# Kernel optimization log

Measured on AMD Instinct MI355X. Metric: run time of the kernel, lower is better.

## Reference

```python
import jax, jax.numpy as jnp
import numpy as np

B, S, DIM, H, DH, DEPTH, NCLS = 4, 2048, 128, 8, 128, 2, 10
M = 128          # number of FAVOR+ random features
CHUNK = 128      # chunk size for causal linear attention
INNER = H * DH   # performer-pytorch: dim_head=dim -> inner_dim = heads*dim
FF = 4 * DIM


def layernorm(x, g, b, eps=1e-5):
    mu = jnp.mean(x, axis=-1, keepdims=True)
    var = jnp.mean((x - mu) ** 2, axis=-1, keepdims=True)
    return (x - mu) * jax.lax.rsqrt(var + eps) * g + b


def softmax_kernel(data, proj, is_query, eps=1e-4):
    # FAVOR+ positive softmax-kernel features. data: [B,H,S,DH], proj: [M,DH]
    norm = DH ** -0.25
    ratio = M ** -0.5
    d = data * norm
    dd = jnp.einsum('bhsd,md->bhsm', d, proj)
    diag = 0.5 * jnp.sum(d * d, axis=-1, keepdims=True)
    if is_query:
        stab = jnp.max(dd, axis=-1, keepdims=True)
    else:
        stab = jnp.max(dd, axis=(-2, -1), keepdims=True)
    stab = jax.lax.stop_gradient(stab)
    return ratio * (jnp.exp(dd - diag - stab) + eps)


def causal_linear_attention(qp, kp, v):
    # qp,kp: [B,H,S,M], v: [B,H,S,DH]; chunked prefix-sum causal linear attention
    b, h, s, m = qp.shape
    d = v.shape[-1]
    nc = s // CHUNK
    def to_chunks(t):
        return t.reshape(b, h, nc, CHUNK, -1).transpose(2, 0, 1, 3, 4)
    qc, kc, vc = to_chunks(qp), to_chunks(kp), to_chunks(v)
    tri = jnp.tril(jnp.ones((CHUNK, CHUNK), qp.dtype))
    def step(carry, inp):
        kv_sum, k_sum = carry           # [b,h,m,d], [b,h,m]
        qi, ki, vi = inp                # [b,h,CHUNK,*]
        attn = jnp.einsum('bhim,bhjm->bhij', qi, ki) * tri
        num = jnp.einsum('bhij,bhjd->bhid', attn, vi) \
            + jnp.einsum('bhim,bhmd->bhid', qi, kv_sum)
        den = jnp.sum(attn, axis=-1) + jnp.einsum('bhim,bhm->bhi', qi, k_sum)
        out = num / (den[..., None] + 1e-6)
        kv_sum = kv_sum + jnp.einsum('bhjm,bhjd->bhmd', ki, vi)
        k_sum = k_sum + jnp.sum(ki, axis=2)
        return (kv_sum, k_sum), out
    init = (jnp.zeros((b, h, m, d), qp.dtype), jnp.zeros((b, h, m), qp.dtype))
    _, out = jax.lax.scan(step, init, (qc, kc, vc))
    return out.transpose(1, 2, 0, 3, 4).reshape(b, h, s, d)


def setup_inputs():
    key = jax.random.key(0)
    ks = jax.random.split(key, 12)
    rng = np.random.default_rng(0)
    # sinusoidal positional encoding [S, DIM]
    pe = np.zeros((S, DIM), np.float32)
    pos = np.arange(S)[:, None].astype(np.float32)
    div = np.exp(np.arange(0, DIM, 2).astype(np.float32) * (-np.log(10000.0) / DIM))
    pe[:, 0::2] = np.sin(pos * div)
    pe[:, 1::2] = np.cos(pos * div)
    # orthogonal random feature projections per layer [DEPTH, M, DH]
    proj = np.stack([
        (np.linalg.qr(rng.standard_normal((DH, DH)))[0][:M] * np.sqrt(DH))
        for _ in range(DEPTH)
    ]).astype(np.float32)
    def gn(k, shape, scale):
        return jax.random.normal(k, shape, jnp.float32) * scale
    return {
        'x': gn(ks[0], (B, S, 1), 1.0),
        'lin_w': gn(ks[1], (1, DIM), 1.0),
        'lin_b': jnp.zeros((DIM,), jnp.float32),
        'pe': jnp.asarray(pe),
        'proj': jnp.asarray(proj),
        'ln1_g': jnp.ones((DEPTH, DIM), jnp.float32),
        'ln1_b': jnp.zeros((DEPTH, DIM), jnp.float32),
        'wq': gn(ks[2], (DEPTH, DIM, INNER), DIM ** -0.5),
        'wk': gn(ks[3], (DEPTH, DIM, INNER), DIM ** -0.5),
        'wv': gn(ks[4], (DEPTH, DIM, INNER), DIM ** -0.5),
        'wo': gn(ks[5], (DEPTH, INNER, DIM), INNER ** -0.5),
        'wo_b': jnp.zeros((DEPTH, DIM), jnp.float32),
        'ln2_g': jnp.ones((DEPTH, DIM), jnp.float32),
        'ln2_b': jnp.zeros((DEPTH, DIM), jnp.float32),
        'ff1_w': gn(ks[6], (DEPTH, DIM, FF), DIM ** -0.5),
        'ff1_b': jnp.zeros((DEPTH, FF), jnp.float32),
        'ff2_w': gn(ks[7], (DEPTH, FF, DIM), FF ** -0.5),
        'ff2_b': jnp.zeros((DEPTH, DIM), jnp.float32),
        'fin_w': gn(ks[8], (DIM, NCLS), DIM ** -0.5),
        'fin_b': jnp.zeros((NCLS,), jnp.float32),
    }


def reference(x, lin_w, lin_b, pe, proj, ln1_g, ln1_b, wq, wk, wv, wo, wo_b,
              ln2_g, ln2_b, ff1_w, ff1_b, ff2_w, ff2_b, fin_w, fin_b):
    h = x @ lin_w + lin_b            # [B,S,DIM]
    h = h + pe[None]
    for l in range(DEPTH):
        # --- pre-norm FAVOR+ causal self-attention ---
        y = layernorm(h, ln1_g[l], ln1_b[l])
        def split(t):  # [B,S,INNER] -> [B,H,S,DH]
            return t.reshape(B, S, H, DH).transpose(0, 2, 1, 3)
        q, k, v = split(y @ wq[l]), split(y @ wk[l]), split(y @ wv[l])
        qp = softmax_kernel(q, proj[l], True)
        kp = softmax_kernel(k, proj[l], False)
        o = causal_linear_attention(qp, kp, v)          # [B,H,S,DH]
        o = o.transpose(0, 2, 1, 3).reshape(B, S, INNER)
        h = h + (o @ wo[l] + wo_b[l])
        # --- pre-norm FFN ---
        y = layernorm(h, ln2_g[l], ln2_b[l])
        f = jax.nn.gelu(y @ ff1_w[l] + ff1_b[l]) @ ff2_w[l] + ff2_b[l]
        h = h + f
    pooled = jnp.mean(h, axis=1)     # [B,DIM]
    return pooled @ fin_w + fin_b    # [B,NCLS]
```

## Files before the change

kernel.cpp:

```cpp
#include <hip/hip_runtime.h>
#include <hip/hip_bf16.h>

#define Bb 4
#define Ss 2048
#define DIMc 128
#define Hh 8
#define DHc 128
#define Mf 128
#define CH 128
#define NCc 16
#define INNERc 1024
#define FFc 512

union F4 { float4 v; float f[4]; };
typedef unsigned short u16;

typedef __bf16 bf16x8 __attribute__((ext_vector_type(8)));
typedef float  f32x4  __attribute__((ext_vector_type(4)));

__device__ __forceinline__ unsigned fkey(float f){
  unsigned b = __float_as_uint(f);
  return (b & 0x80000000u) ? ~b : (b | 0x80000000u);
}
__device__ __forceinline__ float funkey(unsigned u){
  unsigned b = (u & 0x80000000u) ? (u & 0x7fffffffu) : ~u;
  return __uint_as_float(b);
}
__device__ __forceinline__ float gelu_f(float x){
  return 0.5f*x*(1.0f + tanhf(0.7978845608028654f*(x + 0.044715f*x*x*x)));
}
__device__ __forceinline__ u16 f2bu(float f){
  unsigned u = __float_as_uint(f);
  return (u16)((u + 0x7fffu + ((u>>16)&1u)) >> 16);
}
__device__ __forceinline__ float b2f(u16 u){
  return __uint_as_float(((unsigned)u)<<16);
}

__device__ __forceinline__ bf16x8 ldfrag(const u16* base, int row, int e){
  int byte = (row*256 + e*2) ^ ((row&7)<<4);
  return *(const bf16x8*)((const char*)base + byte);
}
__device__ __forceinline__ void stage_lin_bf(u16* dst, const u16* src, int srs, int t){
  #pragma unroll
  for(int it=0; it<8; ++it){
    int idx = t + it*256; int r = idx>>4, c8 = idx&15;
    int byte = (r*256 + c8*16) ^ ((r&7)<<4);
    *(uint4*)((char*)dst + byte) = *(const uint4*)(src + r*srs + c8*8);
  }
}
__device__ __forceinline__ void stage_lin_bf_s(u16* dst, const u16* src, int srs,
    int t, float sc, float off){
  #pragma unroll
  for(int it=0; it<8; ++it){
    int idx = t + it*256; int r = idx>>4, c8 = idx&15;
    u16 tmp[8]; *(uint4*)tmp = *(const uint4*)(src + r*srs + c8*8);
    #pragma unroll
    for(int u=0;u<8;u++) tmp[u] = f2bu(fmaf(b2f(tmp[u]), sc, off));
    int byte = (r*256 + c8*16) ^ ((r&7)<<4);
    *(uint4*)((char*)dst + byte) = *(uint4*)tmp;
  }
}
__device__ __forceinline__ void stage_lin_f32(u16* dst, const float* src, int srs, int t){
  #pragma unroll
  for(int it=0; it<8; ++it){
    int idx = t + it*256; int r = idx>>4, c8 = idx&15;
    F4 v0, v1;
    v0.v = *(const float4*)(src + r*srs + c8*8);
    v1.v = *(const float4*)(src + r*srs + c8*8 + 4);
    u16 tmp[8];
    #pragma unroll
    for(int u=0;u<4;u++){ tmp[u] = f2bu(v0.f[u]); tmp[4+u] = f2bu(v1.f[u]); }
    int byte = (r*256 + c8*16) ^ ((r&7)<<4);
    *(uint4*)((char*)dst + byte) = *(uint4*)tmp;
  }
}
__device__ __forceinline__ void stage_tr_bf(u16* dst, const u16* src, int srs, int t){
  int j0 = (t & 63)*2; int wv = t>>6;
  #pragma unroll
  for(int it=0; it<2; ++it){
    int d0 = wv*16 + it*64;
    u16 a0[16], a1[16];
    *(uint4*)&a0[0] = *(const uint4*)(src + j0*srs + d0);
    *(uint4*)&a0[8] = *(const uint4*)(src + j0*srs + d0 + 8);
    *(uint4*)&a1[0] = *(const uint4*)(src + (j0+1)*srs + d0);
    *(uint4*)&a1[8] = *(const uint4*)(src + (j0+1)*srs + d0 + 8);
    #pragma unroll
    for(int dc=0; dc<16; ++dc){
      int d = d0 + dc;
      unsigned pk = (unsigned)a0[dc] | ((unsigned)a1[dc]<<16);
      int byte = (d*256 + j0*2) ^ ((d&7)<<4);
      *(unsigned*)((char*)dst + byte) = pk;
    }
  }
}
__device__ __forceinline__ void stage_tr_bf_s(u16* dst, const u16* src, int srs,
    int t, float sc, float off){
  int j0 = (t & 63)*2; int wv = t>>6;
  #pragma unroll
  for(int it=0; it<2; ++it){
    int d0 = wv*16 + it*64;
    u16 a0[16], a1[16];
    *(uint4*)&a0[0] = *(const uint4*)(src + j0*srs + d0);
    *(uint4*)&a0[8] = *(const uint4*)(src + j0*srs + d0 + 8);
    *(uint4*)&a1[0] = *(const uint4*)(src + (j0+1)*srs + d0);
    *(uint4*)&a1[8] = *(const uint4*)(src + (j0+1)*srs + d0 + 8);
    #pragma unroll
    for(int dc=0; dc<16; ++dc){
      int d = d0 + dc;
      unsigned pk = (unsigned)f2bu(fmaf(b2f(a0[dc]), sc, off)) |
                    ((unsigned)f2bu(fmaf(b2f(a1[dc]), sc, off))<<16);
      int byte = (d*256 + j0*2) ^ ((d&7)<<4);
      *(unsigned*)((char*)dst + byte) = pk;
    }
  }
}

__device__ __forceinline__ int2 swz_tile(){
  int nx = gridDim.x;
  int nwg = gridDim.x*gridDim.y;
  int lin = blockIdx.y*nx + blockIdx.x;
  int q = nwg>>3, r = nwg&7;
  int xcd = lin&7, idx = lin>>3;
  int nl = (xcd<r) ? (xcd*(q+1)+idx) : (r*(q+1)+(xcd-r)*q+idx);
  return make_int2(nl % nx, nl / nx);
}

__global__ __launch_bounds__(64) void k_init(unsigned* kstab){
  if(threadIdx.x < 64) kstab[threadIdx.x] = 0u;
}

__global__ __launch_bounds__(256) void k_embed(const float* __restrict__ x,
    const float* __restrict__ lw, const float* __restrict__ lb,
    const float* __restrict__ pe, float* __restrict__ h){
  int idx = blockIdx.x*256 + threadIdx.x;
  int d = idx & 127; int bs = idx >> 7; int s = bs & (Ss-1);
  h[idx] = x[bs]*lw[d] + lb[d] + pe[s*DIMc + d];
}

__global__ __launch_bounds__(256) void k_ln(const float* __restrict__ in,
    const float* __restrict__ g, const float* __restrict__ bta,
    u16* __restrict__ out){
  int wave = threadIdx.x >> 6; int lane = threadIdx.x & 63;
  int row = blockIdx.x*4 + wave;
  const float* r = in + row*DIMc;
  float x1 = r[lane], x2 = r[lane+64];
  float s = x1+x2, sq = x1*x1 + x2*x2;
  #pragma unroll
  for(int m=1;m<64;m<<=1){ s += __shfl_xor(s,m,64); sq += __shfl_xor(sq,m,64); }
  float mu = s * (1.0f/128.0f);
  float var = sq*(1.0f/128.0f) - mu*mu;
  float rs = rsqrtf(var + 1e-5f);
  out[row*DIMc+lane]    = f2bu((x1-mu)*rs*g[lane]+bta[lane]);
  out[row*DIMc+lane+64] = f2bu((x2-mu)*rs*g[lane+64]+bta[lane+64]);
}

template<bool QKV3, bool BIAS, bool GELU>
__global__ __launch_bounds__(256) void k_gemm128(const u16* __restrict__ A,
    const float* __restrict__ B0, const float* __restrict__ B1,
    const float* __restrict__ B2, const float* __restrict__ bias,
    u16* __restrict__ C0, u16* __restrict__ C1, u16* __restrict__ C2,
    int N){
  __shared__ __align__(16) u16 As[16384];
  __shared__ __align__(16) u16 Bs[16384];
  int2 tt = swz_tile();
  int tn = tt.x, m0 = tt.y*128;
  const float* Bw; u16* C; int n0;
  if(QKV3){
    int tpw = N>>7;
    int widx = tn / tpw; n0 = (tn % tpw)*128;
    Bw = (widx==0) ? B0 : ((widx==1) ? B1 : B2);
    C  = (widx==0) ? C0 : ((widx==1) ? C1 : C2);
  } else { Bw = B0; C = C0; n0 = tn*128; }
  int t = threadIdx.x; int lane = t&63, w = t>>6;
  int fr = lane&15, kc = lane>>4;
  stage_lin_bf(As, A + (size_t)m0*128, 128, t);
  {
    #pragma unroll
    for(int it=0; it<8; ++it){
      int idx = t + it*256; int n = idx&127, c8 = idx>>7;
      u16 tmp[8];
      #pragma unroll
      for(int j=0;j<8;j++) tmp[j] = f2bu(Bw[(c8*8+j)*N + n0 + n]);
      int byte = (n*256 + c8*16) ^ ((n&7)<<4);
      *(uint4*)((char*)Bs + byte) = *(uint4*)tmp;
    }
  }
  __syncthreads();
  f32x4 acc[2][8] = {};
  #pragma unroll
  for(int ks=0; ks<4; ++ks){
    bf16x8 a[2];
    #pragma unroll
    for(int i=0;i<2;i++) a[i] = ldfrag(As, w*32+i*16+fr, ks*32+kc*8);
    bf16x8 bm[8];
    #pragma unroll
    for(int cb=0;cb<8;cb++) bm[cb] = ldfrag(Bs, cb*16+fr, ks*32+kc*8);
    #pragma unroll
    for(int i=0;i<2;i++)
      #pragma unroll
      for(int cb=0;cb<8;cb++)
        acc[i][cb] = __builtin_amdgcn_mfma_f32_16x16x32_bf16(a[i], bm[cb], acc[i][cb], 0,0,0);
  }
  #pragma unroll
  for(int i=0;i<2;i++){
    #pragma unroll
    for(int r=0;r<4;r++){
      int row = m0 + w*32 + i*16 + kc*4 + r;
      #pragma unroll
      for(int cb=0;cb<8;cb++){
        int col = n0 + cb*16 + fr;
        float val = acc[i][cb][r];
        if(BIAS) val += bias[col];
        if(GELU) val = gelu_f(val);
        C[(size_t)row*N + col] = f2bu(val);
      }
    }
  }
}

template<bool BIAS, bool GELU, bool RES, bool OBF>
__global__ __launch_bounds__(256) void k_gemm_bf(const u16* __restrict__ A,
    const float* __restrict__ Bw, const float* __restrict__ bias,
    const float* __restrict__ resid, void* __restrict__ Cp, int N, int K){
  __shared__ u16 As[64][40];
  __shared__ u16 Bs[64][40];
  int2 tt = swz_tile();
  int n0 = tt.x*64, m0 = tt.y*64;
  int t = threadIdx.x; int wid = t>>6, lane = t&63;
  int wr = wid>>1, wc = wid&1;
  int fr = lane&15, kc = lane>>4;
  f32x4 acc[2][2] = {};
  for(int k0=0; k0<K; k0+=32){
    {
      int r = t>>2, c8 = t&3;
      *(uint4*)&As[r][c8*8] = *(const uint4*)(A + (m0+r)*K + k0 + c8*8);
    }
    {
      int n = t&63, c8 = t>>6;
      u16 tmp[8];
      #pragma unroll
      for(int j=0;j<8;j++) tmp[j] = f2bu(Bw[(k0 + c8*8 + j)*N + n0 + n]);
      *(uint4*)&Bs[n][c8*8] = *(uint4*)tmp;
    }
    __syncthreads();
    bf16x8 af[2], bf[2];
    #pragma unroll
    for(int i=0;i<2;i++) af[i] = *(const bf16x8*)&As[wr*32 + i*16 + fr][kc*8];
    #pragma unroll
    for(int j=0;j<2;j++) bf[j] = *(const bf16x8*)&Bs[wc*32 + j*16 + fr][kc*8];
    #pragma unroll
    for(int i=0;i<2;i++)
      #pragma unroll
      for(int j=0;j<2;j++)
        acc[i][j] = __builtin_amdgcn_mfma_f32_16x16x32_bf16(af[i], bf[j], acc[i][j], 0, 0, 0);
    __syncthreads();
  }
  #pragma unroll
  for(int i=0;i<2;i++){
    #pragma unroll
    for(int r=0;r<4;r++){
      int row = m0 + wr*32 + i*16 + kc*4 + r;
      #pragma unroll
      for(int j=0;j<2;j++){
        int col = n0 + wc*32 + j*16 + fr;
        float val = acc[i][j][r];
        if(BIAS) val += bias[col];
        if(GELU) val = gelu_f(val);
        if(RES)  val += resid[row*N+col];
        if(OBF) ((u16*)Cp)[row*N+col] = f2bu(val);
        else    ((float*)Cp)[row*N+col] = val;
      }
    }
  }
}

__global__ __launch_bounds__(256) void k_featboth(
    u16* __restrict__ qbuf, u16* __restrict__ kbuf,
    const float* __restrict__ proj, unsigned* __restrict__ kstab){
  __shared__ __align__(16) u16 xs[16384];
  __shared__ __align__(16) u16 ps[16384];
  __shared__ float diag_s[128];
  __shared__ unsigned hmax[8];
  int blk = blockIdx.x;
  bool isq = blk < 512;
  int r0 = (blk & 511)*128;
  u16* xin = isq ? qbuf : kbuf;
  int t = threadIdx.x; int lane = t&63, w = t>>6;
  int fr = lane&15, kc = lane>>4;
  const float norm  = 0.29730177875068026f;
  const float ratio = 0.08838834764831845f;
  if(!isq && t<8) hmax[t] = 0u;
  stage_lin_bf(xs, xin + (size_t)r0*128, 128, t);
  stage_lin_f32(ps, proj, 128, t);
  {
    int r = t>>1, half = t&1;
    const u16* rp = xin + (size_t)(r0+r)*128 + half*64;
    float ss = 0.f;
    #pragma unroll
    for(int u4=0; u4<8; ++u4){
      u16 tmp[8]; *(uint4*)tmp = *(const uint4*)(rp + u4*8);
      #pragma unroll
      for(int u=0;u<8;u++){ float f = b2f(tmp[u]); ss += f*f; }
    }
    ss += __shfl_xor(ss, 1, 64);
    if(half==0) diag_s[r] = 0.5f*norm*norm*ss;
  }
  __syncthreads();
  f32x4 acc[2][8] = {};
  #pragma unroll
  for(int ks=0; ks<4; ++ks){
    bf16x8 a[2];
    #pragma unroll
    for(int i=0;i<2;i++) a[i] = ldfrag(xs, w*32+i*16+fr, ks*32+kc*8);
    bf16x8 bm[8];
    #pragma unroll
    for(int cb=0;cb<8;cb++) bm[cb] = ldfrag(ps, cb*16+fr, ks*32+kc*8);
    #pragma unroll
    for(int i=0;i<2;i++)
      #pragma unroll
      for(int cb=0;cb<8;cb++)
        acc[i][cb] = __builtin_amdgcn_mfma_f32_16x16x32_bf16(a[i], bm[cb], acc[i][cb], 0,0,0);
  }
  __syncthreads();
  #pragma unroll
  for(int i=0;i<2;i++){
    #pragma unroll
    for(int r=0;r<4;r++){
      int row = w*32 + i*16 + kc*4 + r;
      float dg = diag_s[row];
      float rmax = acc[i][0][r];
      #pragma unroll
      for(int cb=1;cb<8;cb++) rmax = fmaxf(rmax, acc[i][cb][r]);
      #pragma unroll
      for(int msk=1;msk<16;msk<<=1) rmax = fmaxf(rmax, __shfl_xor(rmax, msk, 64));
      if(isq){
        float base = -dg - norm*rmax;
        #pragma unroll
        for(int cb=0;cb<8;cb++){
          float val = ratio*(expf(fmaf(norm, acc[i][cb][r], base)) + 1e-4f);
          int byte = (row*256 + (cb*16+fr)*2) ^ ((row&7)<<4);
          *(u16*)((char*)xs + byte) = f2bu(val);
        }
      } else {
        if(fr==0) atomicMax(&hmax[row&7], fkey(norm*rmax));
        #pragma unroll
        for(int cb=0;cb<8;cb++){
          float val = expf(fmaf(norm, acc[i][cb][r], -dg));
          int byte = (row*256 + (cb*16+fr)*2) ^ ((row&7)<<4);
          *(u16*)((char*)xs + byte) = f2bu(val);
        }
      }
    }
  }
  __syncthreads();
  #pragma unroll
  for(int it=0; it<8; ++it){
    int idx = t + it*256; int r = idx>>4, c8 = idx&15;
    int byte = (r*256 + c8*16) ^ ((r&7)<<4);
    *(uint4*)(xin + (size_t)(r0+r)*128 + c8*8) = *(uint4*)((char*)xs + byte);
  }
  if(!isq){
    int b = r0 >> 14;
    if(t<8) atomicMax(&kstab[b*8 + t], hmax[t]);
  }
}

__global__ __launch_bounds__(256) void k_attn1m(const u16* __restrict__ kp,
    const u16* __restrict__ v, u16* __restrict__ kvc, float* __restrict__ ksc,
    const unsigned* __restrict__ kstab){
  __shared__ __align__(16) u16 kt[16384];
  __shared__ __align__(16) u16 vt[16384];
  int bc = blockIdx.x; int c = bc&15, bh = bc>>4, b = bh>>3, hh = bh&7;
  int t = threadIdx.x; int lane = t&63, w = t>>6;
  int fr = lane&15, kc = lane>>4;
  int s0 = c*128;
  const float ratio = 0.08838834764831845f;
  float stab = funkey(kstab[bh]);
  float csc = ratio * expf(-stab);
  float reps = ratio * 1e-4f;
  const u16* kb = kp + (size_t)((b*Ss+s0)*Hh + hh)*128;
  const u16* vb = v  + (size_t)((b*Ss+s0)*Hh + hh)*128;
  stage_tr_bf_s(kt, kb, 1024, t, csc, reps);
  stage_tr_bf(vt, vb, 1024, t);
  __syncthreads();
  f32x4 acc[2][8] = {};
  f32x4 ks[2] = {};
  bf16x8 bones;
  #pragma unroll
  for(int e=0;e<8;e++) bones[e] = (fr==0) ? (__bf16)1.0f : (__bf16)0.0f;
  #pragma unroll
  for(int js=0;js<4;js++){
    bf16x8 am[2];
    #pragma unroll
    for(int i=0;i<2;i++) am[i] = ldfrag(kt, w*32+i*16+fr, js*32+kc*8);
    bf16x8 bv[8];
    #pragma unroll
    for(int cb=0;cb<8;cb++) bv[cb] = ldfrag(vt, cb*16+fr, js*32+kc*8);
    #pragma unroll
    for(int i=0;i<2;i++){
      ks[i] = __builtin_amdgcn_mfma_f32_16x16x32_bf16(am[i], bones, ks[i], 0,0,0);
      #pragma unroll
      for(int cb=0;cb<8;cb++)
        acc[i][cb] = __builtin_amdgcn_mfma_f32_16x16x32_bf16(am[i], bv[cb], acc[i][cb], 0,0,0);
    }
  }
  u16* kvb = kvc + (size_t)bc*16384;
  #pragma unroll
  for(int i=0;i<2;i++){
    #pragma unroll
    for(int r=0;r<4;r++){
      int m = w*32 + i*16 + kc*4 + r;
      #pragma unroll
      for(int cb=0;cb<8;cb++) kvb[m*128 + cb*16 + fr] = f2bu(acc[i][cb][r]);
      if(fr==0) ksc[bc*128 + m] = ks[i][r];
    }
  }
}

__global__ __launch_bounds__(256) void k_prefix2(unsigned* __restrict__ kvc,
    float* __restrict__ ksc){
  int blk = blockIdx.x;
  if(blk < 1024){
    int bh = blk >> 5; int pos = (blk & 31)*256 + threadIdx.x;
    int base = bh*16*8192 + pos;
    float a0 = 0.f, a1 = 0.f;
    #pragma unroll
    for(int c=0;c<16;c++){
      unsigned pk = kvc[base + c*8192];
      float x0 = b2f((u16)pk), x1 = b2f((u16)(pk>>16));
      kvc[base + c*8192] = (unsigned)f2bu(a0) | ((unsigned)f2bu(a1)<<16);
      a0 += x0; a1 += x1;
    }
  } else {
    int e = (blk-1024)*256 + threadIdx.x;
    int bh = e>>7, m = e&127;
    float a = 0.f;
    #pragma unroll
    for(int c=0;c<16;c++){
      int idx = (bh*16+c)*128 + m;
      float xv = ksc[idx]; ksc[idx] = a; a += xv;
    }
  }
}

__global__ __launch_bounds__(256) void k_attn2m(const u16* __restrict__ qp,
    const u16* __restrict__ kp, const u16* __restrict__ v,
    const u16* __restrict__ kvc, const float* __restrict__ ksc,
    u16* __restrict__ o, const unsigned* __restrict__ kstab){
  __shared__ __align__(16) u16 qs[16384];
  __shared__ __align__(16) u16 bs[16384];
  __shared__ float ksum_s[128];
  int bc = blockIdx.x; int c = bc&15, bh = bc>>4, b = bh>>3, hh = bh&7;
  int t = threadIdx.x; int lane = t&63, w = t>>6;
  int fr = lane&15, kc = lane>>4;
  int s0 = c*128;
  const float ratio = 0.08838834764831845f;
  float stab = funkey(kstab[bh]);
  float csc = ratio * expf(-stab);
  float reps = ratio * 1e-4f;
  const u16* qb = qp + (size_t)((b*Ss+s0)*Hh + hh)*128;
  const u16* kb = kp + (size_t)((b*Ss+s0)*Hh + hh)*128;
  const u16* vb = v  + (size_t)((b*Ss+s0)*Hh + hh)*128;
  const u16* kvb = kvc + (size_t)bc*16384;
  stage_lin_bf(qs, qb, 1024, t);
  stage_lin_bf_s(bs, kb, 1024, t, csc, reps);
  if(t<128) ksum_s[t] = ksc[bc*128 + t];
  __syncthreads();
  bf16x8 aq[2][4];
  #pragma unroll
  for(int i=0;i<2;i++)
    #pragma unroll
    for(int ks=0;ks<4;ks++)
      aq[i][ks] = ldfrag(qs, w*32+i*16+fr, ks*32+kc*8);
  f32x4 sacc[2][8] = {};
  #pragma unroll
  for(int ks=0;ks<4;ks++){
    bf16x8 bk[8];
    #pragma unroll
    for(int cb=0;cb<8;cb++) bk[cb] = ldfrag(bs, cb*16+fr, ks*32+kc*8);
    #pragma unroll
    for(int i=0;i<2;i++)
      #pragma unroll
      for(int cb=0;cb<8;cb++)
        sacc[i][cb] = __builtin_amdgcn_mfma_f32_16x16x32_bf16(aq[i][ks], bk[cb], sacc[i][cb], 0,0,0);
  }
  __syncthreads();
  #pragma unroll
  for(int i=0;i<2;i++){
    #pragma unroll
    for(int cb=0;cb<8;cb++){
      #pragma unroll
      for(int r=0;r<4;r++){
        int prow = w*32 + i*16 + kc*4 + r;
        int pcol = cb*16 + fr;
        float pv = (pcol > prow) ? 0.f : sacc[i][cb][r];
        int byte = (prow*256 + pcol*2) ^ ((prow&7)<<4);
        *(u16*)((char*)qs + byte) = f2bu(pv);
      }
    }
  }
  stage_tr_bf(bs, vb, 1024, t);
  __syncthreads();
  f32x4 nacc[2][8] = {};
  f32x4 dacc[2] = {};
  bf16x8 bones;
  #pragma unroll
  for(int e=0;e<8;e++) bones[e] = (fr==0) ? (__bf16)1.0f : (__bf16)0.0f;
  #pragma unroll
  for(int js=0;js<4;js++){
    bf16x8 ap[2];
    #pragma unroll
    for(int i=0;i<2;i++) ap[i] = ldfrag(qs, w*32+i*16+fr, js*32+kc*8);
    bf16x8 bv[8];
    #pragma unroll
    for(int cb=0;cb<8;cb++) bv[cb] = ldfrag(bs, cb*16+fr, js*32+kc*8);
    #pragma unroll
    for(int i=0;i<2;i++){
      dacc[i] = __builtin_amdgcn_mfma_f32_16x16x32_bf16(ap[i], bones, dacc[i], 0,0,0);
      #pragma unroll
      for(int cb=0;cb<8;cb++)
        nacc[i][cb] = __builtin_amdgcn_mfma_f32_16x16x32_bf16(ap[i], bv[cb], nacc[i][cb], 0,0,0);
    }
  }
  __syncthreads();
  stage_tr_bf(bs, kvb, 128, t);
  __syncthreads();
  #pragma unroll
  for(int ms=0;ms<4;ms++){
    bf16x8 bkv[8];
    #pragma unroll
    for(int cb=0;cb<8;cb++) bkv[cb] = ldfrag(bs, cb*16+fr, ms*32+kc*8);
    bf16x8 bks;
    #pragma unroll
    for(int e=0;e<8;e++) bks[e] = (fr==0) ? (__bf16)ksum_s[ms*32+kc*8+e] : (__bf16)0.0f;
    #pragma unroll
    for(int i=0;i<2;i++){
      dacc[i] = __builtin_amdgcn_mfma_f32_16x16x32_bf16(aq[i][ms], bks, dacc[i], 0,0,0);
      #pragma unroll
      for(int cb=0;cb<8;cb++)
        nacc[i][cb] = __builtin_amdgcn_mfma_f32_16x16x32_bf16(aq[i][ms], bkv[cb], nacc[i][cb], 0,0,0);
    }
  }
  #pragma unroll
  for(int i=0;i<2;i++){
    #pragma unroll
    for(int r=0;r<4;r++){
      float den = __shfl(dacc[i][r], lane & 48, 64);
      float inv = 1.0f/(den + 1e-6f);
      int row = w*32 + i*16 + kc*4 + r;
      u16* ob = o + (size_t)((b*Ss+s0+row)*Hh + hh)*128;
      #pragma unroll
      for(int cb=0;cb<8;cb++)
        ob[cb*16 + fr] = f2bu(nacc[i][cb][r] * inv);
    }
  }
}

__global__ __launch_bounds__(256) void k_pool(const float* __restrict__ h,
    float* __restrict__ pw){
  __shared__ float part[256];
  int blk = blockIdx.x; int b = blk>>4, c = blk&15;
  int t = threadIdx.x; int half = t>>7;
  float s = 0.f;
  int s0 = c*128 + half*64;
  for(int si=s0; si<s0+64; ++si) s += h[(b*Ss+si)*128 + (t&127)];
  part[t] = s;
  __syncthreads();
  if(t<128) pw[blk*128 + t] = part[t] + part[t+128];
}
__global__ __launch_bounds__(128) void k_cls(const float* __restrict__ pw,
    const float* __restrict__ fw, const float* __restrict__ fb,
    float* __restrict__ out){
  __shared__ float pool_s[128];
  int b = blockIdx.x; int t = threadIdx.x;
  float s = 0.f;
  for(int c=0;c<16;c++) s += pw[(b*16+c)*128 + t];
  pool_s[t] = s * (1.0f/2048.0f);
  __syncthreads();
  if(t<10){
    float a = fb[t];
    for(int d=0; d<128; ++d) a += pool_s[d]*fw[d*10+t];
    out[b*10+t] = a;
  }
}

extern "C" void kernel_launch(void* const* d_in, const int* in_sizes, int n_in,
                              void* d_out, int out_size, void* d_ws, size_t ws_size,
                              hipStream_t stream){
  (void)in_sizes; (void)n_in; (void)out_size; (void)ws_size;
  const float* x     = (const float*)d_in[0];
  const float* lin_w = (const float*)d_in[1];
  const float* lin_b = (const float*)d_in[2];
  const float* pe    = (const float*)d_in[3];
  const float* proj  = (const float*)d_in[4];
  const float* ln1_g = (const float*)d_in[5];
  const float* ln1_b = (const float*)d_in[6];
  const float* wq    = (const float*)d_in[7];
  const float* wk    = (const float*)d_in[8];
  const float* wv    = (const float*)d_in[9];
  const float* wo    = (const float*)d_in[10];
  const float* wo_b  = (const float*)d_in[11];
  const float* ln2_g = (const float*)d_in[12];
  const float* ln2_b = (const float*)d_in[13];
  const float* ff1w  = (const float*)d_in[14];
  const float* ff1b  = (const float*)d_in[15];
  const float* ff2w  = (const float*)d_in[16];
  const float* ff2b  = (const float*)d_in[17];
  const float* finw  = (const float*)d_in[18];
  const float* finb  = (const float*)d_in[19];
  float* out = (float*)d_out;

  float* ws  = (float*)d_ws;
  float* h    = ws;
  u16*  y    = (u16*)(h + 1048576);
  u16*  q    = (u16*)(h + 1048576 + 524288);
  u16*  k    = q + 8388608;
  u16*  v    = k + 8388608;
  u16*  o    = v + 8388608;
  u16*  kvc  = o + 8388608;
  float* ksc  = (float*)(kvc + 8388608);
  float* pw   = ksc + 65536;
  unsigned* kstab = (unsigned*)(pw + 8192);

  k_init<<<1,64,0,stream>>>(kstab);
  k_embed<<<4096,256,0,stream>>>(x, lin_w, lin_b, pe, h);
  for(int l=0;l<2;l++){
    const float* projl = proj + l*Mf*DHc;
    k_ln<<<2048,256,0,stream>>>(h, ln1_g + l*DIMc, ln1_b + l*DIMc, y);
    k_gemm128<true,false,false><<<dim3(24,64),256,0,stream>>>(
        y, wq + l*DIMc*INNERc, wk + l*DIMc*INNERc, wv + l*DIMc*INNERc,
        nullptr, q, k, v, INNERc);
    k_featboth<<<1024,256,0,stream>>>(q, k, projl, kstab + l*32);
    k_attn1m<<<512,256,0,stream>>>(k, v, kvc, ksc, kstab + l*32);
    k_prefix2<<<1040,256,0,stream>>>((unsigned*)kvc, ksc);
    k_attn2m<<<512,256,0,stream>>>(q, k, v, kvc, ksc, o, kstab + l*32);
    k_gemm_bf<true,false,true,false><<<dim3(2,128),256,0,stream>>>(o, wo + l*INNERc*DIMc, wo_b + l*DIMc, h, h, DIMc, INNERc);
    k_ln<<<2048,256,0,stream>>>(h, ln2_g + l*DIMc, ln2_b + l*DIMc, y);
    k_gemm128<false,true,true><<<dim3(4,64),256,0,stream>>>(
        y, ff1w + l*DIMc*FFc, nullptr, nullptr, ff1b + l*FFc,
        q, nullptr, nullptr, FFc);
    k_gemm_bf<true,false,true,false><<<dim3(2,128),256,0,stream>>>(q, ff2w + l*FFc*DIMc, ff2b + l*DIMc, h, h, DIMc, FFc);
  }
  k_pool<<<64,256,0,stream>>>(h, pw);
  k_cls<<<4,128,0,stream>>>(pw, finw, finb, out);
}
```

Before: 439.6 us.

## Pre-transpose output/FF2 weights to bf16 and use LDS-free direct-load GEMM

A prep kernel converts and transposes the wo and ff2 weights to bf16 once per call. The output-projection and FF2 GEMMs then load MFMA operands straight from global memory with no LDS staging and no barriers, and add the result into the residual in place. The k_init launch is folded into k_embed to save one launch. This removes per-tile fp32 strided weight loads and conversions, plus the sync overhead, but adds an extra prep launch and relies on cache reuse for the direct global loads.

After: 408.5 us. -7.1%, faster.

```diff
diff --git a/kernel.cpp b/kernel.cpp
--- a/kernel.cpp
+++ b/kernel.cpp
@@ -126,16 +126,28 @@
   return make_int2(nl % nx, nl / nx);
 }
 
-__global__ __launch_bounds__(64) void k_init(unsigned* kstab){
-  if(threadIdx.x < 64) kstab[threadIdx.x] = 0u;
-}
-
 __global__ __launch_bounds__(256) void k_embed(const float* __restrict__ x,
     const float* __restrict__ lw, const float* __restrict__ lb,
-    const float* __restrict__ pe, float* __restrict__ h){
+    const float* __restrict__ pe, float* __restrict__ h,
+    unsigned* __restrict__ kstab){
+  if(blockIdx.x==0 && threadIdx.x<64) kstab[threadIdx.x] = 0u;
   int idx = blockIdx.x*256 + threadIdx.x;
   int d = idx & 127; int bs = idx >> 7; int s = bs & (Ss-1);
   h[idx] = x[bs]*lw[d] + lb[d] + pe[s*DIMc + d];
+}
+
+__global__ __launch_bounds__(256) void k_prep(const float* __restrict__ wo,
+    const float* __restrict__ ff2, u16* __restrict__ woT, u16* __restrict__ ff2T){
+  int blk = blockIdx.x;
+  if(blk < 1024){
+    int idx = blk*256 + threadIdx.x;
+    int k = idx & 1023; int n = (idx>>10) & 127; int l = idx>>17;
+    woT[idx] = f2bu(wo[l*131072 + k*128 + n]);
+  } else {
+    int idx = (blk-1024)*256 + threadIdx.x;
+    int k = idx & 511; int n = (idx>>9) & 127; int l = idx>>16;
+    ff2T[idx] = f2bu(ff2[l*65536 + k*128 + n]);
+  }
 }
 
 __global__ __launch_bounds__(256) void k_ln(const float* __restrict__ in,
@@ -219,42 +231,29 @@
   }
 }
 
-template<bool BIAS, bool GELU, bool RES, bool OBF>
-__global__ __launch_bounds__(256) void k_gemm_bf(const u16* __restrict__ A,
-    const float* __restrict__ Bw, const float* __restrict__ bias,
-    const float* __restrict__ resid, void* __restrict__ Cp, int N, int K){
-  __shared__ u16 As[64][40];
-  __shared__ u16 Bs[64][40];
+__global__ __launch_bounds__(256) void k_gemm_direct(const u16* __restrict__ A,
+    const u16* __restrict__ BT, const float* __restrict__ bias,
+    float* __restrict__ C, int N, int K){
   int2 tt = swz_tile();
   int n0 = tt.x*64, m0 = tt.y*64;
   int t = threadIdx.x; int wid = t>>6, lane = t&63;
   int wr = wid>>1, wc = wid&1;
   int fr = lane&15, kc = lane>>4;
+  const u16* a0p = A  + (size_t)(m0+wr*32+fr)*K    + kc*8;
+  const u16* a1p = A  + (size_t)(m0+wr*32+16+fr)*K + kc*8;
+  const u16* b0p = BT + (size_t)(n0+wc*32+fr)*K    + kc*8;
+  const u16* b1p = BT + (size_t)(n0+wc*32+16+fr)*K + kc*8;
   f32x4 acc[2][2] = {};
+  #pragma unroll 4
   for(int k0=0; k0<K; k0+=32){
-    {
-      int r = t>>2, c8 = t&3;
-      *(uint4*)&As[r][c8*8] = *(const uint4*)(A + (m0+r)*K + k0 + c8*8);
-    }
-    {
-      int n = t&63, c8 = t>>6;
-      u16 tmp[8];
-      #pragma unroll
-      for(int j=0;j<8;j++) tmp[j] = f2bu(Bw[(k0 + c8*8 + j)*N + n0 + n]);
-      *(uint4*)&Bs[n][c8*8] = *(uint4*)tmp;
-    }
-    __syncthreads();
-    bf16x8 af[2], bf[2];
-    #pragma unroll
-    for(int i=0;i<2;i++) af[i] = *(const bf16x8*)&As[wr*32 + i*16 + fr][kc*8];
-    #pragma unroll
-    for(int j=0;j<2;j++) bf[j] = *(const bf16x8*)&Bs[wc*32 + j*16 + fr][kc*8];
-    #pragma unroll
-    for(int i=0;i<2;i++)
-      #pragma unroll
-      for(int j=0;j<2;j++)
-        acc[i][j] = __builtin_amdgcn_mfma_f32_16x16x32_bf16(af[i], bf[j], acc[i][j], 0, 0, 0);
-    __syncthreads();
+    bf16x8 af0 = *(const bf16x8*)(a0p + k0);
+    bf16x8 af1 = *(const bf16x8*)(a1p + k0);
+    bf16x8 bf0 = *(const bf16x8*)(b0p + k0);
+    bf16x8 bf1 = *(const bf16x8*)(b1p + k0);
+    acc[0][0] = __builtin_amdgcn_mfma_f32_16x16x32_bf16(af0, bf0, acc[0][0], 0,0,0);
+    acc[0][1] = __builtin_amdgcn_mfma_f32_16x16x32_bf16(af0, bf1, acc[0][1], 0,0,0);
+    acc[1][0] = __builtin_amdgcn_mfma_f32_16x16x32_bf16(af1, bf0, acc[1][0], 0,0,0);
+    acc[1][1] = __builtin_amdgcn_mfma_f32_16x16x32_bf16(af1, bf1, acc[1][1], 0,0,0);
   }
   #pragma unroll
   for(int i=0;i<2;i++){
@@ -264,12 +263,8 @@
       #pragma unroll
       for(int j=0;j<2;j++){
         int col = n0 + wc*32 + j*16 + fr;
-        float val = acc[i][j][r];
-        if(BIAS) val += bias[col];
-        if(GELU) val = gelu_f(val);
-        if(RES)  val += resid[row*N+col];
-        if(OBF) ((u16*)Cp)[row*N+col] = f2bu(val);
-        else    ((float*)Cp)[row*N+col] = val;
+        float val = acc[i][j][r] + bias[col];
+        C[(size_t)row*N+col] += val;
       }
     }
   }
@@ -622,9 +617,11 @@
   float* ksc  = (float*)(kvc + 8388608);
   float* pw   = ksc + 65536;
   unsigned* kstab = (unsigned*)(pw + 8192);
-
-  k_init<<<1,64,0,stream>>>(kstab);
-  k_embed<<<4096,256,0,stream>>>(x, lin_w, lin_b, pe, h);
+  u16*  woT  = (u16*)(kstab + 64);
+  u16*  ff2T = woT + 262144;
+
+  k_embed<<<4096,256,0,stream>>>(x, lin_w, lin_b, pe, h, kstab);
+  k_prep<<<1536,256,0,stream>>>(wo, ff2w, woT, ff2T);
   for(int l=0;l<2;l++){
     const float* projl = proj + l*Mf*DHc;
     k_ln<<<2048,256,0,stream>>>(h, ln1_g + l*DIMc, ln1_b + l*DIMc, y);
@@ -635,12 +632,12 @@
     k_attn1m<<<512,256,0,stream>>>(k, v, kvc, ksc, kstab + l*32);
     k_prefix2<<<1040,256,0,stream>>>((unsigned*)kvc, ksc);
     k_attn2m<<<512,256,0,stream>>>(q, k, v, kvc, ksc, o, kstab + l*32);
-    k_gemm_bf<true,false,true,false><<<dim3(2,128),256,0,stream>>>(o, wo + l*INNERc*DIMc, wo_b + l*DIMc, h, h, DIMc, INNERc);
+    k_gemm_direct<<<dim3(2,128),256,0,stream>>>(o, woT + l*131072, wo_b + l*DIMc, h, DIMc, INNERc);
     k_ln<<<2048,256,0,stream>>>(h, ln2_g + l*DIMc, ln2_b + l*DIMc, y);
     k_gemm128<false,true,true><<<dim3(4,64),256,0,stream>>>(
         y, ff1w + l*DIMc*FFc, nullptr, nullptr, ff1b + l*FFc,
         q, nullptr, nullptr, FFc);
-    k_gemm_bf<true,false,true,false><<<dim3(2,128),256,0,stream>>>(q, ff2w + l*FFc*DIMc, ff2b + l*DIMc, h, h, DIMc, FFc);
+    k_gemm_direct<<<dim3(2,128),256,0,stream>>>(q, ff2T + l*65536, ff2b + l*DIMc, h, DIMc, FFc);
   }
   k_pool<<<64,256,0,stream>>>(h, pw);
   k_cls<<<4,128,0,stream>>>(pw, finw, finb, out);
```
